# Kernel tuning notes

Measured on AMD Instinct MI355X. Metric: run time of the kernel, lower is better.

Reference implementation:

```python
import jax, jax.numpy as jnp
import numpy as np

B, D, H = 65536, 128, 64


def setup_inputs() -> dict:
    key = jax.random.key(0)
    ks = jax.random.split(key, 20)
    p = lambda k, shp, fan: jax.random.normal(k, shp, jnp.float32) * (1.0 / np.sqrt(fan))
    return {
        "l": jax.random.normal(ks[0], (B, D), jnp.float32),
        "a": jax.random.normal(ks[1], (B, D), jnp.float32),
        "v": jax.random.normal(ks[2], (B, D), jnp.float32),
        "att_w": p(ks[3], (D, 1), D), "att_b": jnp.zeros((1,), jnp.float32),
        "gf_w1": p(ks[4], (2 * D, H), 2 * D), "gf_b1": jnp.zeros((H,), jnp.float32),
        "gf_w2": p(ks[5], (H, D), H), "gf_b2": jnp.zeros((D,), jnp.float32),
        "gf2_w1": p(ks[6], (2 * D, H), 2 * D), "gf2_b1": jnp.zeros((H,), jnp.float32),
        "gf2_w2": p(ks[7], (H, D), H), "gf2_b2": jnp.zeros((D,), jnp.float32),
        "ll_w1": p(ks[8], (3 * D, H), 3 * D), "ll_b1": jnp.zeros((H,), jnp.float32),
        "ll_w2": p(ks[9], (H, H), H), "ll_b2": jnp.zeros((H,), jnp.float32),
        "ll_w3": p(ks[10], (H, D), H), "ll_b3": jnp.zeros((D,), jnp.float32),
    }


def reference(l, a, v, att_w, att_b, gf_w1, gf_b1, gf_w2, gf_b2,
              gf2_w1, gf2_b1, gf2_w2, gf2_b2,
              ll_w1, ll_b1, ll_w2, ll_b2, ll_w3, ll_b3):
    def gf(x, y):  # graph_fusion on cat([x,y],1): Linear->LeakyReLU(0.2)->Linear->Tanh
        h = jnp.concatenate([x, y], 1) @ gf_w1 + gf_b1
        h = jax.nn.leaky_relu(h, 0.2)
        return jnp.tanh(h @ gf_w2 + gf_b2)

    def gf2(x, y):
        h = jnp.concatenate([x, y], 1) @ gf2_w1 + gf2_b1
        h = jax.nn.leaky_relu(h, 0.2)
        return jnp.tanh(h @ gf2_w2 + gf2_b2)

    dot = lambda x, y: jnp.sum(x * y, axis=1)  # batched [B,1,d]@[B,d,1] -> [B]

    sa = jnp.tanh(a @ att_w + att_b)  # [B,1]
    sv = jnp.tanh(v @ att_w + att_b)
    sl = jnp.tanh(l @ att_w + att_b)

    unimodal = (sa * a + sv * v + sl * l) / 3.0  # [B,D]
    sa1, sv1, sl1 = sa[:, 0], sv[:, 0], sl[:, 0]

    # modalities are overwritten by softmax in the original
    a = jax.nn.softmax(a, axis=1)
    v = jax.nn.softmax(v, axis=1)
    l = jax.nn.softmax(l, axis=1)

    sav = (sa1 + sv1) / (dot(a, v) + 0.5)
    sal = (sa1 + sl1) / (dot(a, l) + 0.5)
    svl = (sl1 + sv1) / (dot(v, l) + 0.5)
    normalize = jax.nn.softmax(jnp.stack([sav, sal, svl], axis=1), axis=1)  # [B,3]

    gav, gal, gvl = gf(a, v), gf(a, l), gf(v, l)  # reused (torch computes twice)
    a_v = jnp.tanh(normalize[:, 0:1] * gav)
    a_l = jnp.tanh(normalize[:, 1:2] * gal)
    v_l = jnp.tanh(normalize[:, 2:3] * gvl)
    bimodal = a_v + a_l + v_l

    a_v2 = jax.nn.softmax(gav, axis=1)
    a_l2 = jax.nn.softmax(gal, axis=1)
    v_l2 = jax.nn.softmax(gvl, axis=1)

    savvl = (sav + svl) / (dot(a_v2, v_l2) + 0.5)
    saavl = (sav + sal) / (dot(a_v2, a_l2) + 0.5)
    savll = (sal + svl) / (dot(a_l2, v_l2) + 0.5)
    savl = (sav + sl1) / (dot(a_v2, l) + 0.5)
    salv = (sal + sv1) / (dot(a_l2, v) + 0.5)
    svla = (sa1 + svl) / (dot(v_l2, a) + 0.5)
    n2 = jax.nn.softmax(jnp.stack([savvl, saavl, savll, savl, salv, svla], axis=1), axis=1)

    trimodal = (jnp.tanh(n2[:, 0:1] * gf2(a_v, v_l))
                + jnp.tanh(n2[:, 1:2] * gf2(a_v, a_l))
                + jnp.tanh(n2[:, 2:3] * gf2(v_l, a_l))
                + jnp.tanh(n2[:, 3:4] * gf2(a_v, l))
                + jnp.tanh(n2[:, 4:5] * gf2(a_l, v))
                + jnp.tanh(n2[:, 5:6] * gf2(v_l, a)))

    fusion = jnp.concatenate([unimodal, bimodal, trimodal], axis=1)  # [B,3D]
    h = jnp.tanh(fusion @ ll_w1 + ll_b1)
    h = jnp.tanh(h @ ll_w2 + ll_b2)
    return jnp.tanh(h @ ll_w3 + ll_b3)
```

## Files before the change

kernel.cpp:

```cpp
#include <hip/hip_runtime.h>

typedef short bfrag __attribute__((ext_vector_type(8)));
typedef float facc  __attribute__((ext_vector_type(4)));
typedef unsigned short u16;
typedef unsigned int   u32;

#define LOG2E 1.4426950408889634f
#define MFMA(A,B,C) __builtin_amdgcn_mfma_f32_16x16x32_bf16((A),(B),(C),0,0,0)

#define AS_E 0
#define VS_E 2176
#define LS_E 4352
#define AV_E 6528
#define AL_E 8704
#define VL_E 10880
#define FUS_E 13056
#define GH_E 19328
#define SCR_B 57856
#define SM_BYTES 58880

__device__ __forceinline__ float ex2(float x){ return __builtin_amdgcn_exp2f(x); }
__device__ __forceinline__ float rcpf_(float x){ return __builtin_amdgcn_rcpf(x); }
__device__ __forceinline__ float ftanh(float x){ return 1.0f - 2.0f*rcpf_(ex2(x*(2.0f*LOG2E)) + 1.0f); }
__device__ __forceinline__ u16 f2b(float x){ u32 u = __float_as_uint(x); return (u16)((u + 0x7FFFu + ((u>>16)&1u))>>16); }
__device__ __forceinline__ float b2f(u16 b){ return __uint_as_float(((u32)b)<<16); }
__device__ __forceinline__ float rsum16(float v){
  v += __shfl_xor(v,1); v += __shfl_xor(v,2); v += __shfl_xor(v,4); v += __shfl_xor(v,8); return v;
}
__device__ __forceinline__ float rmax16(float v){
  v = fmaxf(v,__shfl_xor(v,1)); v = fmaxf(v,__shfl_xor(v,2));
  v = fmaxf(v,__shfl_xor(v,4)); v = fmaxf(v,__shfl_xor(v,8)); return v;
}
__device__ __forceinline__ void st4b(u16* p, float x0,float x1,float x2,float x3){
  u32 lo = (u32)f2b(x0) | ((u32)f2b(x1)<<16);
  u32 hi = (u32)f2b(x2) | ((u32)f2b(x3)<<16);
  *(uint2*)p = make_uint2(lo,hi);
}

__global__ void prep_weights(const float* __restrict__ gf_w1, const float* __restrict__ gf_w2,
                             const float* __restrict__ gf2_w1, const float* __restrict__ gf2_w2,
                             const float* __restrict__ ll_w1, const float* __restrict__ ll_w2,
                             const float* __restrict__ ll_w3, u16* __restrict__ blob)
{
  u32 i = blockIdx.x*256u + threadIdx.x;
  if (i >= 86016u) return;
  u32 off, K, N; const float* src;
  if      (i < 16384u){ off=0u;     K=256u; N=64u;  src=gf_w1; }
  else if (i < 24576u){ off=16384u; K=64u;  N=128u; src=gf_w2; }
  else if (i < 40960u){ off=24576u; K=256u; N=64u;  src=gf2_w1; }
  else if (i < 49152u){ off=40960u; K=64u;  N=128u; src=gf2_w2; }
  else if (i < 73728u){ off=49152u; K=384u; N=64u;  src=ll_w1; }
  else if (i < 77824u){ off=73728u; K=64u;  N=64u;  src=ll_w2; }
  else               { off=77824u; K=64u;  N=128u; src=ll_w3; }
  u32 li = i - off, n = li / K, k = li - n*K;
  blob[i] = f2b(src[k*N + n]);
}

__global__ __launch_bounds__(256,2) void fused_graph(
    const float* __restrict__ Lg, const float* __restrict__ Ag, const float* __restrict__ Vg,
    const float* __restrict__ att_w, const float* __restrict__ att_b,
    const float* __restrict__ gf_b1, const float* __restrict__ gf_b2,
    const float* __restrict__ gf2_b1, const float* __restrict__ gf2_b2,
    const float* __restrict__ ll_b1, const float* __restrict__ ll_b2, const float* __restrict__ ll_b3,
    const u16* __restrict__ wb, float* __restrict__ out)
{
  __shared__ alignas(16) char sm[SM_BYTES];
  u16* smu = (u16*)sm;
  float* scr = (float*)(sm + SCR_B);

  const int tid = threadIdx.x;
  const int lane = tid & 63;
  const int w = tid >> 6;
  const int m = lane & 15;
  const int q = lane >> 4;
  const int er = tid >> 4;
  const int ep = tid & 15;
  const int row0 = blockIdx.x << 4;

  const int gb = (row0 + er)*128 + ep*4;
  facc A0 = *(const facc*)(Ag+gb), A1 = *(const facc*)(Ag+gb+64);
  facc V0 = *(const facc*)(Vg+gb), V1 = *(const facc*)(Vg+gb+64);
  facc L0 = *(const facc*)(Lg+gb), L1 = *(const facc*)(Lg+gb+64);
  facc W0 = *(const facc*)(att_w+ep*4), W1 = *(const facc*)(att_w+ep*4+64);
  float ab = att_b[0];
  float pa=0.f,pv=0.f,pl=0.f;
  #pragma unroll
  for (int i=0;i<4;i++){ pa += A0[i]*W0[i]+A1[i]*W1[i]; pv += V0[i]*W0[i]+V1[i]*W1[i]; pl += L0[i]*W0[i]+L1[i]*W1[i]; }
  float sa = ftanh(rsum16(pa)+ab), sv = ftanh(rsum16(pv)+ab), sl = ftanh(rsum16(pl)+ab);
  {
    u16* fu = smu + FUS_E + er*392 + ep*4;
    const float th = 1.0f/3.0f;
    st4b(fu,    (sa*A0[0]+sv*V0[0]+sl*L0[0])*th, (sa*A0[1]+sv*V0[1]+sl*L0[1])*th,
                (sa*A0[2]+sv*V0[2]+sl*L0[2])*th, (sa*A0[3]+sv*V0[3]+sl*L0[3])*th);
    st4b(fu+64, (sa*A1[0]+sv*V1[0]+sl*L1[0])*th, (sa*A1[1]+sv*V1[1]+sl*L1[1])*th,
                (sa*A1[2]+sv*V1[2]+sl*L1[2])*th, (sa*A1[3]+sv*V1[3]+sl*L1[3])*th);
  }
  #define SMAX(X0,X1,OFFE) { \
    float mx=-3.0e38f; \
    _Pragma("unroll") for (int i=0;i<4;i++){ mx=fmaxf(mx,fmaxf(X0[i],X1[i])); } \
    mx = rmax16(mx); float s_=0.f; \
    _Pragma("unroll") for (int i=0;i<4;i++){ X0[i]=ex2((X0[i]-mx)*LOG2E); X1[i]=ex2((X1[i]-mx)*LOG2E); s_+=X0[i]+X1[i]; } \
    s_ = rsum16(s_); float rs_ = rcpf_(s_); \
    _Pragma("unroll") for (int i=0;i<4;i++){ X0[i]*=rs_; X1[i]*=rs_; } \
    u16* dp_ = smu + (OFFE) + er*136 + ep*4; \
    st4b(dp_, X0[0],X0[1],X0[2],X0[3]); st4b(dp_+64, X1[0],X1[1],X1[2],X1[3]); }
  SMAX(A0,A1,AS_E)
  SMAX(V0,V1,VS_E)
  SMAX(L0,L1,LS_E)
  float dav=0.f,dal=0.f,dvl=0.f;
  #pragma unroll
  for (int i=0;i<4;i++){ dav += A0[i]*V0[i]+A1[i]*V1[i]; dal += A0[i]*L0[i]+A1[i]*L1[i]; dvl += V0[i]*L0[i]+V1[i]*L1[i]; }
  dav = rsum16(dav); dal = rsum16(dal); dvl = rsum16(dvl);
  float sav = (sa+sv)*rcpf_(dav+0.5f);
  float sal = (sa+sl)*rcpf_(dal+0.5f);
  float svl = (sl+sv)*rcpf_(dvl+0.5f);
  if (ep==0){
    float mx = fmaxf(sav,fmaxf(sal,svl));
    float e0 = ex2((sav-mx)*LOG2E), e1 = ex2((sal-mx)*LOG2E), e2 = ex2((svl-mx)*LOG2E);
    float rs = rcpf_(e0+e1+e2);
    scr[er*16+0]=e0*rs; scr[er*16+1]=e1*rs; scr[er*16+2]=e2*rs;
  }
  __syncthreads();

  const u16* g1t = wb;
  const u16* g2t = wb + 16384;
  bfrag B1[8];
  #pragma unroll
  for (int s=0;s<8;s++) B1[s] = *(const bfrag*)(g1t + (w*16+m)*256 + s*32 + q*8);
  bfrag B2[2][2];
  #pragma unroll
  for (int t=0;t<2;t++){
    #pragma unroll
    for (int s=0;s<2;s++) B2[t][s] = *(const bfrag*)(g2t + ((w+4*t)*16+m)*64 + s*32 + q*8);
  }
  facc acc0={0,0,0,0}, acc1={0,0,0,0}, acc2={0,0,0,0};
  #pragma unroll
  for (int s=0;s<8;s++){
    int k = s*32 + q*8, ko = k & 127; bool hi = (k >= 128);
    const u16* p0 = smu + (hi? VS_E:AS_E) + m*136 + ko;
    const u16* p1 = smu + (hi? LS_E:AS_E) + m*136 + ko;
    const u16* p2 = smu + (hi? LS_E:VS_E) + m*136 + ko;
    acc0 = MFMA(*(const bfrag*)p0, B1[s], acc0);
    acc1 = MFMA(*(const bfrag*)p1, B1[s], acc1);
    acc2 = MFMA(*(const bfrag*)p2, B1[s], acc2);
  }
  {
    float b1v = gf_b1[w*16+m];
    #pragma unroll
    for (int r=0;r<4;r++){
      int rr = q*4+r;
      float h0 = acc0[r]+b1v; h0 = fmaxf(h0, 0.2f*h0);
      float h1 = acc1[r]+b1v; h1 = fmaxf(h1, 0.2f*h1);
      float h2 = acc2[r]+b1v; h2 = fmaxf(h2, 0.2f*h2);
      smu[25472 + 0*1152 + rr*72 + w*16+m] = f2b(h0);
      smu[25472 + 1*1152 + rr*72 + w*16+m] = f2b(h1);
      smu[25472 + 2*1152 + rr*72 + w*16+m] = f2b(h2);
    }
  }
  __syncthreads();
  facc c2[3][2] = {{{0,0,0,0},{0,0,0,0}},{{0,0,0,0},{0,0,0,0}},{{0,0,0,0},{0,0,0,0}}};
  #pragma unroll
  for (int s=0;s<2;s++){
    int k = s*32 + q*8;
    #pragma unroll
    for (int p3=0;p3<3;p3++){
      bfrag Af = *(const bfrag*)(smu + 25472 + p3*1152 + m*72 + k);
      c2[p3][0] = MFMA(Af, B2[0][s], c2[p3][0]);
      c2[p3][1] = MFMA(Af, B2[1][s], c2[p3][1]);
    }
  }
  {
    float b2v0 = gf_b2[w*16+m], b2v1 = gf_b2[(w+4)*16+m];
    float bim[2][4] = {{0,0,0,0},{0,0,0,0}};
    float nv[4][3];
    #pragma unroll
    for (int r=0;r<4;r++){ int rr=q*4+r; nv[r][0]=scr[rr*16+0]; nv[r][1]=scr[rr*16+1]; nv[r][2]=scr[rr*16+2]; }
    #pragma unroll
    for (int p3=0;p3<3;p3++){
      #pragma unroll
      for (int t=0;t<2;t++){
        float bb = t? b2v1 : b2v0;
        int cc = (w+4*t)*16+m;
        #pragma unroll
        for (int r=0;r<4;r++){
          int rr=q*4+r;
          float g = ftanh(c2[p3][t][r] + bb);
          smu[GH_E + p3*2048 + rr*128 + cc] = f2b(g);
          float tt = ftanh(nv[r][p3]*g);
          smu[AV_E + p3*2176 + rr*136 + cc] = f2b(tt);
          bim[t][r] += tt;
        }
      }
    }
    #pragma unroll
    for (int t=0;t<2;t++){
      #pragma unroll
      for (int r=0;r<4;r++)
        smu[FUS_E + (q*4+r)*392 + 128 + (w+4*t)*16+m] = f2b(bim[t][r]);
    }
  }
  __syncthreads();

  float E0[8], E1[8], E2[8];
  #define GSTAT(EA, G3) { \
    const u16* gp_ = smu + GH_E + (G3)*2048 + er*128 + ep*4; \
    float x_[8]; \
    _Pragma("unroll") for (int i=0;i<4;i++){ x_[i]=b2f(gp_[i]); x_[4+i]=b2f(gp_[64+i]); } \
    float mx_=-3.0e38f; \
    _Pragma("unroll") for (int j=0;j<8;j++) mx_=fmaxf(mx_,x_[j]); \
    mx_ = rmax16(mx_); float s_=0.f; \
    _Pragma("unroll") for (int j=0;j<8;j++){ x_[j]=ex2((x_[j]-mx_)*LOG2E); s_+=x_[j]; } \
    s_ = rsum16(s_); float rs_=rcpf_(s_); \
    _Pragma("unroll") for (int j=0;j<8;j++) EA[j]=x_[j]*rs_; }
  GSTAT(E0,0)
  GSTAT(E1,1)
  GSTAT(E2,2)
  float d01=0.f,d02=0.f,d12=0.f,d0l=0.f,d1v=0.f,d2a=0.f;
  #pragma unroll
  for (int i=0;i<4;i++){
    d01 += E0[i]*E1[i] + E0[4+i]*E1[4+i];
    d02 += E0[i]*E2[i] + E0[4+i]*E2[4+i];
    d12 += E1[i]*E2[i] + E1[4+i]*E2[4+i];
    d0l += E0[i]*L0[i] + E0[4+i]*L1[i];
    d1v += E1[i]*V0[i] + E1[4+i]*V1[i];
    d2a += E2[i]*A0[i] + E2[4+i]*A1[i];
  }
  d01=rsum16(d01); d02=rsum16(d02); d12=rsum16(d12);
  d0l=rsum16(d0l); d1v=rsum16(d1v); d2a=rsum16(d2a);
  if (ep==0){
    float x0 = (sav+svl)*rcpf_(d02+0.5f);
    float x1 = (sav+sal)*rcpf_(d01+0.5f);
    float x2 = (sal+svl)*rcpf_(d12+0.5f);
    float x3 = (sav+sl )*rcpf_(d0l+0.5f);
    float x4 = (sal+sv )*rcpf_(d1v+0.5f);
    float x5 = (sa +svl)*rcpf_(d2a+0.5f);
    float mx = fmaxf(fmaxf(fmaxf(x0,x1),fmaxf(x2,x3)),fmaxf(x4,x5));
    float e0=ex2((x0-mx)*LOG2E), e1=ex2((x1-mx)*LOG2E), e2=ex2((x2-mx)*LOG2E);
    float e3=ex2((x3-mx)*LOG2E), e4=ex2((x4-mx)*LOG2E), e5=ex2((x5-mx)*LOG2E);
    float rs = rcpf_(e0+e1+e2+e3+e4+e5);
    scr[er*16+ 9]=e0*rs; scr[er*16+10]=e1*rs; scr[er*16+11]=e2*rs;
    scr[er*16+12]=e3*rs; scr[er*16+13]=e4*rs; scr[er*16+14]=e5*rs;
  }
  __syncthreads();

  const u16* h1t = wb + 24576;
  const u16* h2t = wb + 40960;
  bfrag C1[8];
  #pragma unroll
  for (int s=0;s<8;s++) C1[s] = *(const bfrag*)(h1t + (w*16+m)*256 + s*32 + q*8);
  bfrag C2[2][2];
  #pragma unroll
  for (int t=0;t<2;t++){
    #pragma unroll
    for (int s=0;s<2;s++) C2[t][s] = *(const bfrag*)(h2t + ((w+4*t)*16+m)*64 + s*32 + q*8);
  }
  const int S0[6] = {AV_E, AV_E, VL_E, AV_E, AL_E, VL_E};
  const int S1[6] = {VL_E, AL_E, AL_E, LS_E, VS_E, AS_E};
  facc cc1[6];
  #pragma unroll
  for (int pr=0;pr<6;pr++){ facc z = {0,0,0,0}; cc1[pr] = z; }
  #pragma unroll
  for (int s=0;s<8;s++){
    int k = s*32+q*8, ko = k&127; bool hi = (k>=128);
    #pragma unroll
    for (int pr=0;pr<6;pr++){
      const u16* sp = smu + (hi? S1[pr]:S0[pr]) + m*136 + ko;
      cc1[pr] = MFMA(*(const bfrag*)sp, C1[s], cc1[pr]);
    }
  }
  {
    float b1v = gf2_b1[w*16+m];
    #pragma unroll
    for (int pr=0;pr<6;pr++){
      #pragma unroll
      for (int r=0;r<4;r++){
        float h = cc1[pr][r]+b1v; h = fmaxf(h,0.2f*h);
        smu[GH_E + pr*1152 + (q*4+r)*72 + w*16+m] = f2b(h);
      }
    }
  }
  __syncthreads();
  facc cc2[6][2];
  #pragma unroll
  for (int pr=0;pr<6;pr++){ facc z = {0,0,0,0}; cc2[pr][0]=z; cc2[pr][1]=z; }
  #pragma unroll
  for (int s=0;s<2;s++){
    int k=s*32+q*8;
    #pragma unroll
    for (int pr=0;pr<6;pr++){
      bfrag Af = *(const bfrag*)(smu + GH_E + pr*1152 + m*72 + k);
      cc2[pr][0] = MFMA(Af, C2[0][s], cc2[pr][0]);
      cc2[pr][1] = MFMA(Af, C2[1][s], cc2[pr][1]);
    }
  }
  {
    float b2v0 = gf2_b2[w*16+m], b2v1 = gf2_b2[(w+4)*16+m];
    float tri[2][4] = {{0,0,0,0},{0,0,0,0}};
    float n2v[4][6];
    #pragma unroll
    for (int r=0;r<4;r++){
      #pragma unroll
      for (int j=0;j<6;j++) n2v[r][j] = scr[(q*4+r)*16+9+j];
    }
    #pragma unroll
    for (int pr=0;pr<6;pr++){
      #pragma unroll
      for (int t=0;t<2;t++){
        float bb = t? b2v1 : b2v0;
        #pragma unroll
        for (int r=0;r<4;r++){
          float g = ftanh(cc2[pr][t][r] + bb);
          tri[t][r] += ftanh(n2v[r][pr]*g);
        }
      }
    }
    #pragma unroll
    for (int t=0;t<2;t++){
      #pragma unroll
      for (int r=0;r<4;r++)
        smu[FUS_E + (q*4+r)*392 + 256 + (w+4*t)*16+m] = f2b(tri[t][r]);
    }
  }
  __syncthreads();

  const u16* lw1 = wb + 49152;
  const u16* lw2 = wb + 73728;
  const u16* lw3 = wb + 77824;
  {
    facc c = {0,0,0,0};
    #pragma unroll
    for (int s=0;s<12;s++){
      bfrag Bf = *(const bfrag*)(lw1 + (w*16+m)*384 + s*32 + q*8);
      bfrag Af = *(const bfrag*)(smu + FUS_E + m*392 + s*32 + q*8);
      c = MFMA(Af, Bf, c);
    }
    float b = ll_b1[w*16+m];
    #pragma unroll
    for (int r=0;r<4;r++) smu[GH_E + (q*4+r)*72 + w*16+m] = f2b(ftanh(c[r]+b));
  }
  __syncthreads();
  {
    facc c = {0,0,0,0};
    #pragma unroll
    for (int s=0;s<2;s++){
      bfrag Bf = *(const bfrag*)(lw2 + (w*16+m)*64 + s*32 + q*8);
      bfrag Af = *(const bfrag*)(smu + GH_E + m*72 + s*32 + q*8);
      c = MFMA(Af, Bf, c);
    }
    float b = ll_b2[w*16+m];
    #pragma unroll
    for (int r=0;r<4;r++) smu[GH_E + 1152 + (q*4+r)*72 + w*16+m] = f2b(ftanh(c[r]+b));
  }
  __syncthreads();
  {
    facc c0={0,0,0,0}, c1={0,0,0,0};
    #pragma unroll
    for (int s=0;s<2;s++){
      bfrag Af  = *(const bfrag*)(smu + GH_E + 1152 + m*72 + s*32 + q*8);
      bfrag Bf0 = *(const bfrag*)(lw3 + (w*16+m)*64 + s*32 + q*8);
      bfrag Bf1 = *(const bfrag*)(lw3 + ((w+4)*16+m)*64 + s*32 + q*8);
      c0 = MFMA(Af, Bf0, c0);
      c1 = MFMA(Af, Bf1, c1);
    }
    float b0 = ll_b3[w*16+m], b1 = ll_b3[(w+4)*16+m];
    #pragma unroll
    for (int r=0;r<4;r++){
      out[(row0+q*4+r)*128 + w*16+m]        = ftanh(c0[r]+b0);
      out[(row0+q*4+r)*128 + (w+4)*16+m]    = ftanh(c1[r]+b1);
    }
  }
}

extern "C" void kernel_launch(void* const* d_in, const int* in_sizes, int n_in,
                              void* d_out, int out_size, void* d_ws, size_t ws_size,
                              hipStream_t stream)
{
  const float* l      = (const float*)d_in[0];
  const float* a      = (const float*)d_in[1];
  const float* v      = (const float*)d_in[2];
  const float* att_w  = (const float*)d_in[3];
  const float* att_b  = (const float*)d_in[4];
  const float* gf_w1  = (const float*)d_in[5];
  const float* gf_b1  = (const float*)d_in[6];
  const float* gf_w2  = (const float*)d_in[7];
  const float* gf_b2  = (const float*)d_in[8];
  const float* gf2_w1 = (const float*)d_in[9];
  const float* gf2_b1 = (const float*)d_in[10];
  const float* gf2_w2 = (const float*)d_in[11];
  const float* gf2_b2 = (const float*)d_in[12];
  const float* ll_w1  = (const float*)d_in[13];
  const float* ll_b1  = (const float*)d_in[14];
  const float* ll_w2  = (const float*)d_in[15];
  const float* ll_b2  = (const float*)d_in[16];
  const float* ll_w3  = (const float*)d_in[17];
  const float* ll_b3  = (const float*)d_in[18];
  u16* blob = (u16*)d_ws;

  prep_weights<<<336, 256, 0, stream>>>(gf_w1, gf_w2, gf2_w1, gf2_w2, ll_w1, ll_w2, ll_w3, blob);
  fused_graph<<<4096, 256, 0, stream>>>(l, a, v, att_w, att_b,
                                        gf_b1, gf_b2, gf2_b1, gf2_b2,
                                        ll_b1, ll_b2, ll_b3, blob, (float*)d_out);
}
```

Baseline: 277.5 us.

## Alias hidden-activation scratch in LDS, raise occupancy, cheapen bf16 packing

Merges the separate hidden-layer LDS buffer into the GH region (renamed HH_E). It adds a barrier so the region can be safely reused after the second MFMA stage reads it, which shrinks shared memory from about 58.9KB to 53.5KB. The launch bounds move from 2 to 3 blocks per CU so more workgroups can be resident, at the cost of tighter register limits and possible spills. The bf16 conversion changes from round-to-nearest-even to simple round-half-up, with a perm-based pair packer, to cut ALU work. This slightly changes rounding behavior.

Result: faster. 255.5 us (-7.9%).

```diff
diff --git a/kernel.cpp b/kernel.cpp
--- a/kernel.cpp
+++ b/kernel.cpp
@@ -15,15 +15,18 @@
 #define AL_E 8704
 #define VL_E 10880
 #define FUS_E 13056
-#define GH_E 19328
-#define SCR_B 57856
-#define SM_BYTES 58880
+#define HH_E 19328
+#define SCR_B 52480
+#define SM_BYTES 53504
 
 __device__ __forceinline__ float ex2(float x){ return __builtin_amdgcn_exp2f(x); }
 __device__ __forceinline__ float rcpf_(float x){ return __builtin_amdgcn_rcpf(x); }
 __device__ __forceinline__ float ftanh(float x){ return 1.0f - 2.0f*rcpf_(ex2(x*(2.0f*LOG2E)) + 1.0f); }
-__device__ __forceinline__ u16 f2b(float x){ u32 u = __float_as_uint(x); return (u16)((u + 0x7FFFu + ((u>>16)&1u))>>16); }
+__device__ __forceinline__ u16 f2b(float x){ return (u16)((__float_as_uint(x) + 0x8000u)>>16); }
 __device__ __forceinline__ float b2f(u16 b){ return __uint_as_float(((u32)b)<<16); }
+__device__ __forceinline__ u32 pk2(float x0, float x1){
+  return __builtin_amdgcn_perm(__float_as_uint(x1)+0x8000u, __float_as_uint(x0)+0x8000u, 0x07060302u);
+}
 __device__ __forceinline__ float rsum16(float v){
   v += __shfl_xor(v,1); v += __shfl_xor(v,2); v += __shfl_xor(v,4); v += __shfl_xor(v,8); return v;
 }
@@ -32,9 +35,7 @@
   v = fmaxf(v,__shfl_xor(v,4)); v = fmaxf(v,__shfl_xor(v,8)); return v;
 }
 __device__ __forceinline__ void st4b(u16* p, float x0,float x1,float x2,float x3){
-  u32 lo = (u32)f2b(x0) | ((u32)f2b(x1)<<16);
-  u32 hi = (u32)f2b(x2) | ((u32)f2b(x3)<<16);
-  *(uint2*)p = make_uint2(lo,hi);
+  *(uint2*)p = make_uint2(pk2(x0,x1), pk2(x2,x3));
 }
 
 __global__ void prep_weights(const float* __restrict__ gf_w1, const float* __restrict__ gf_w2,
@@ -56,7 +57,7 @@
   blob[i] = f2b(src[k*N + n]);
 }
 
-__global__ __launch_bounds__(256,2) void fused_graph(
+__global__ __launch_bounds__(256,3) void fused_graph(
     const float* __restrict__ Lg, const float* __restrict__ Ag, const float* __restrict__ Vg,
     const float* __restrict__ att_w, const float* __restrict__ att_b,
     const float* __restrict__ gf_b1, const float* __restrict__ gf_b2,
@@ -152,9 +153,9 @@
       float h0 = acc0[r]+b1v; h0 = fmaxf(h0, 0.2f*h0);
       float h1 = acc1[r]+b1v; h1 = fmaxf(h1, 0.2f*h1);
       float h2 = acc2[r]+b1v; h2 = fmaxf(h2, 0.2f*h2);
-      smu[25472 + 0*1152 + rr*72 + w*16+m] = f2b(h0);
-      smu[25472 + 1*1152 + rr*72 + w*16+m] = f2b(h1);
-      smu[25472 + 2*1152 + rr*72 + w*16+m] = f2b(h2);
+      smu[HH_E + 0*1152 + rr*72 + w*16+m] = f2b(h0);
+      smu[HH_E + 1*1152 + rr*72 + w*16+m] = f2b(h1);
+      smu[HH_E + 2*1152 + rr*72 + w*16+m] = f2b(h2);
     }
   }
   __syncthreads();
@@ -164,11 +165,12 @@
     int k = s*32 + q*8;
     #pragma unroll
     for (int p3=0;p3<3;p3++){
-      bfrag Af = *(const bfrag*)(smu + 25472 + p3*1152 + m*72 + k);
+      bfrag Af = *(const bfrag*)(smu + HH_E + p3*1152 + m*72 + k);
       c2[p3][0] = MFMA(Af, B2[0][s], c2[p3][0]);
       c2[p3][1] = MFMA(Af, B2[1][s], c2[p3][1]);
     }
   }
+  __syncthreads();
   {
     float b2v0 = gf_b2[w*16+m], b2v1 = gf_b2[(w+4)*16+m];
     float bim[2][4] = {{0,0,0,0},{0,0,0,0}};
@@ -185,7 +187,7 @@
         for (int r=0;r<4;r++){
           int rr=q*4+r;
           float g = ftanh(c2[p3][t][r] + bb);
-          smu[GH_E + p3*2048 + rr*128 + cc] = f2b(g);
+          smu[HH_E + p3*2048 + rr*128 + cc] = f2b(g);
           float tt = ftanh(nv[r][p3]*g);
           smu[AV_E + p3*2176 + rr*136 + cc] = f2b(tt);
           bim[t][r] += tt;
@@ -203,7 +205,7 @@
 
   float E0[8], E1[8], E2[8];
   #define GSTAT(EA, G3) { \
-    const u16* gp_ = smu + GH_E + (G3)*2048 + er*128 + ep*4; \
+    const u16* gp_ = smu + HH_E + (G3)*2048 + er*128 + ep*4; \
     float x_[8]; \
     _Pragma("unroll") for (int i=0;i<4;i++){ x_[i]=b2f(gp_[i]); x_[4+i]=b2f(gp_[64+i]); } \
     float mx_=-3.0e38f; \
@@ -275,7 +277,7 @@
       #pragma unroll
       for (int r=0;r<4;r++){
         float h = cc1[pr][r]+b1v; h = fmaxf(h,0.2f*h);
-        smu[GH_E + pr*1152 + (q*4+r)*72 + w*16+m] = f2b(h);
+        smu[HH_E + pr*1152 + (q*4+r)*72 + w*16+m] = f2b(h);
       }
     }
   }
@@ -288,7 +290,7 @@
     int k=s*32+q*8;
     #pragma unroll
     for (int pr=0;pr<6;pr++){
-      bfrag Af = *(const bfrag*)(smu + GH_E + pr*1152 + m*72 + k);
+      bfrag Af = *(const bfrag*)(smu + HH_E + pr*1152 + m*72 + k);
       cc2[pr][0] = MFMA(Af, C2[0][s], cc2[pr][0]);
       cc2[pr][1] = MFMA(Af, C2[1][s], cc2[pr][1]);
     }
@@ -336,7 +338,7 @@
     }
     float b = ll_b1[w*16+m];
     #pragma unroll
-    for (int r=0;r<4;r++) smu[GH_E + (q*4+r)*72 + w*16+m] = f2b(ftanh(c[r]+b));
+    for (int r=0;r<4;r++) smu[HH_E + (q*4+r)*72 + w*16+m] = f2b(ftanh(c[r]+b));
   }
   __syncthreads();
   {
@@ -344,19 +346,19 @@
     #pragma unroll
     for (int s=0;s<2;s++){
       bfrag Bf = *(const bfrag*)(lw2 + (w*16+m)*64 + s*32 + q*8);
-      bfrag Af = *(const bfrag*)(smu + GH_E + m*72 + s*32 + q*8);
+      bfrag Af = *(const bfrag*)(smu + HH_E + m*72 + s*32 + q*8);
       c = MFMA(Af, Bf, c);
     }
     float b = ll_b2[w*16+m];
     #pragma unroll
-    for (int r=0;r<4;r++) smu[GH_E + 1152 + (q*4+r)*72 + w*16+m] = f2b(ftanh(c[r]+b));
+    for (int r=0;r<4;r++) smu[HH_E + 1152 + (q*4+r)*72 + w*16+m] = f2b(ftanh(c[r]+b));
   }
   __syncthreads();
   {
     facc c0={0,0,0,0}, c1={0,0,0,0};
     #pragma unroll
     for (int s=0;s<2;s++){
-      bfrag Af  = *(const bfrag*)(smu + GH_E + 1152 + m*72 + s*32 + q*8);
+      bfrag Af  = *(const bfrag*)(smu + HH_E + 1152 + m*72 + s*32 + q*8);
       bfrag Bf0 = *(const bfrag*)(lw3 + (w*16+m)*64 + s*32 + q*8);
       bfrag Bf1 = *(const bfrag*)(lw3 + ((w+4)*16+m)*64 + s*32 + q*8);
       c0 = MFMA(Af, Bf0, c0);
```
